# Kernel optimization log

Measured on AMD Instinct MI355X. Metric: run time of the kernel, lower is better.

Reference implementation:

```python
import jax, jax.numpy as jnp
import numpy as np
from jax import lax

# ---- config (matches init_kwargs) ----
B, S = 8, 256
WIDTH, LEVELS, STATE, PARAM = 32, 3, 1, 1
WSIZE = (64, 64)
PAD = 1  # padding//2 with padding=2

# ---- db6 filters (pywt ordering) ----
L = 12
DEC_LO = np.array([-0.00107730108499558, 0.004777257511010651, 0.0005538422009938016,
                   -0.031582039318031156, 0.02752286553001629, 0.09750160558707936,
                   -0.12976686756709563, -0.22626469396516913, 0.3152503517092432,
                   0.7511339080215775, 0.4946238903983854, 0.11154074335008017],
                  dtype=np.float32)
REC_LO = DEC_LO[::-1].copy()
REC_HI = ((-1.0) ** np.arange(L)).astype(np.float32) * DEC_LO
DEC_HI = REC_HI[::-1].copy()
# correlation kernels: analysis = flipped dec filters (= rec), synthesis = flipped rec (= dec)
KA = jnp.asarray(np.stack([REC_LO, REC_HI]))   # [2, L]
KS = jnp.asarray(np.stack([DEC_LO, DEC_HI]))   # [2, L]


def dwt1d(x, axis):
    """Single-level analysis along axis (2 or 3) of NCHW x; symmetric pad + stride-2 conv.
    Matches pytorch_wavelets afb1d (symmetric mode, even N)."""
    b, c = x.shape[0], x.shape[1]
    pads = [(0, 0)] * 4
    pads[axis] = (L - 2, L - 2)
    xp = jnp.pad(x, pads, mode='symmetric')
    xr = xp.reshape((b * c, 1) + xp.shape[2:])
    if axis == 2:
        k = KA.reshape(2, 1, L, 1); strides = (2, 1)
    else:
        k = KA.reshape(2, 1, 1, L); strides = (1, 2)
    y = lax.conv_general_dilated(xr, k, strides, 'VALID')  # [b*c, 2, H', W']
    y = y.reshape((b, c, 2) + y.shape[2:])
    return y[:, :, 0], y[:, :, 1]


def idwt1d(lo, hi, axis):
    """Single-level synthesis along axis: zero-upsample (lhs_dilation=2) + conv, crop L-2.
    Matches pytorch_wavelets sfb1d (conv_transpose stride 2, padding L-2)."""
    b, c = lo.shape[0], lo.shape[1]
    x = jnp.stack([lo, hi], axis=2).reshape((b * c, 2) + lo.shape[2:])
    if axis == 2:
        k = KS.reshape(1, 2, L, 1); ld = (2, 1); pad = ((1, 1), (0, 0))
    else:
        k = KS.reshape(1, 2, 1, L); ld = (1, 2); pad = ((0, 0), (1, 1))
    y = lax.conv_general_dilated(x, k, (1, 1), pad, lhs_dilation=ld)  # len = 2N-L+2
    return y.reshape((b, c) + y.shape[2:])


def afb2d(x):
    xl, xh = dwt1d(x, 3)
    ll, lh = dwt1d(xl, 2)
    hl, hh = dwt1d(xh, 2)
    return ll, jnp.stack([lh, hl, hh], axis=2)  # [B,C,3,H',W']


def sfb2d(ll, yh):
    lh, hl, hh = yh[:, :, 0], yh[:, :, 1], yh[:, :, 2]
    xl = idwt1d(ll, lh, 2)
    xh = idwt1d(hl, hh, 2)
    return idwt1d(xl, xh, 3)


def interp_bilinear(w, Ho, Wo):
    """F.interpolate(mode='bilinear', align_corners=False) on [I,O,h,w]."""
    h, wd = w.shape[2], w.shape[3]
    if (h, wd) == (Ho, Wo):
        return w
    def coords(n_out, n_in):
        scale = n_in / n_out
        s = jnp.maximum((jnp.arange(n_out, dtype=jnp.float32) + 0.5) * scale - 0.5, 0.0)
        i0 = jnp.minimum(jnp.floor(s).astype(jnp.int32), n_in - 1)
        i1 = jnp.minimum(i0 + 1, n_in - 1)
        t = jnp.clip(s - i0.astype(jnp.float32), 0.0, 1.0)
        return i0, i1, t
    y0, y1, ty = coords(Ho, h)
    x0, x1, tx = coords(Wo, wd)
    wr = w[:, :, y0, :] * (1.0 - ty)[None, None, :, None] + w[:, :, y1, :] * ty[None, None, :, None]
    return wr[:, :, :, x0] * (1.0 - tx) + wr[:, :, :, x1] * tx


def wavelet_conv(x, w):
    """WaveletConv2d.forward: J-level DWT, per-subband channel mix, IDWT."""
    orig = x.shape
    ll, highs = x, []
    for _ in range(LEVELS):
        ll, yh = afb2d(ll)
        highs.append(yh)
    wi = interp_bilinear(w, ll.shape[-2], ll.shape[-1])
    out = jnp.einsum('bixy,ioxy->boxy', ll, wi)
    out_h = []
    for h in highs:
        # torch code interpolates weights to input.shape[-3:-1] == (3, Hj) and broadcasts over W
        whi = interp_bilinear(w, h.shape[-3], h.shape[-2])
        out_h.append(jnp.einsum('bixyz,ioxy->boxyz', h, whi))
    for h in reversed(out_h):
        out = out[:, :, :h.shape[-2], :h.shape[-1]]
        out = sfb2d(out, h)
    return out[:, :, :orig[2], :orig[3]]


def wno2d(u, par, x, y, fc0_w, fc0_b, wc_w, pw_w, pw_b, fc1_w, fc1_b, fc2_w, fc2_b):
    b, s0, s1 = u.shape[0], u.shape[1], u.shape[2]
    gridx = jnp.broadcast_to(x[:, :, None, None], (b, s0, s1, 1))
    gridy = jnp.broadcast_to(y[:, None, :, None], (b, s0, s1, 1))
    h = jnp.concatenate([u, par, gridx, gridy], axis=-1)      # [B,S0,S1,4]
    h = h @ fc0_w.T + fc0_b                                   # [B,S0,S1,width]
    h = jnp.transpose(h, (0, 3, 1, 2))                        # NCHW
    h = jnp.pad(h, ((0, 0), (0, 0), (PAD, PAD), (PAD, PAD)), mode='reflect')
    for i in range(4):
        u1 = wavelet_conv(h, wc_w[i])
        u2 = jnp.einsum('bixy,oi->boxy', h, pw_w[i]) + pw_b[i][None, :, None, None]
        h = u1 + u2
        if i < 3:
            h = jax.nn.gelu(h, approximate=False)
    h = h[:, :, PAD:-PAD, PAD:-PAD]
    h = jnp.transpose(h, (0, 2, 3, 1))
    h = jax.nn.gelu(h @ fc1_w.T + fc1_b, approximate=False)
    return h @ fc2_w.T + fc2_b                                # [B,S0,S1,state]


def setup_inputs() -> dict:
    key = jax.random.key(0)
    ks = jax.random.split(key, 16)
    f32 = jnp.float32
    scale = 1.0 / (WIDTH * WIDTH)
    return {
        'u': jax.random.normal(ks[0], (B, S, S, STATE), f32),
        'par': jax.random.normal(ks[1], (B, S, S, PARAM), f32),
        'x': jax.random.uniform(ks[2], (B, S), f32),
        'y': jax.random.uniform(ks[3], (B, S), f32),
        'fc0_w': 0.3 * jax.random.normal(ks[4], (WIDTH, STATE + PARAM + 2), f32),
        'fc0_b': jnp.zeros((WIDTH,), f32),
        'wc_w': scale * jax.random.uniform(ks[5], (4, WIDTH, WIDTH) + WSIZE, f32),
        'pw_w': (1.0 / np.sqrt(WIDTH)) * jax.random.normal(ks[6], (4, WIDTH, WIDTH), f32),
        'pw_b': jnp.zeros((4, WIDTH), f32),
        'fc1_w': (1.0 / np.sqrt(WIDTH)) * jax.random.normal(ks[7], (128, WIDTH), f32),
        'fc1_b': jnp.zeros((128,), f32),
        'fc2_w': (1.0 / np.sqrt(128.0)) * jax.random.normal(ks[8], (STATE, 128), f32),
        'fc2_b': jnp.zeros((STATE,), f32),
    }


def reference(u, par, x, y, fc0_w, fc0_b, wc_w, pw_w, pw_b, fc1_w, fc1_b, fc2_w, fc2_b):
    return wno2d(u, par, x, y, fc0_w, fc0_b, wc_w, pw_w, pw_b, fc1_w, fc1_b, fc2_w, fc2_b)
```

## Files before the change

### kernel.cpp

```cpp
#include <hip/hip_runtime.h>
#include <math.h>

#define W0f  (-0.00107730108499558f)
#define W1f  (0.004777257511010651f)
#define W2f  (0.0005538422009938016f)
#define W3f  (-0.031582039318031156f)
#define W4f  (0.02752286553001629f)
#define W5f  (0.09750160558707936f)
#define W6f  (-0.12976686756709563f)
#define W7f  (-0.22626469396516913f)
#define W8f  (0.3152503517092432f)
#define W9f  (0.7511339080215775f)
#define W10f (0.4946238903983854f)
#define W11f (0.11154074335008017f)

__constant__ float cKA0[12] = {W11f,W10f,W9f,W8f,W7f,W6f,W5f,W4f,W3f,W2f,W1f,W0f};
__constant__ float cKA1[12] = {W0f,-W1f,W2f,-W3f,W4f,-W5f,W6f,-W7f,W8f,-W9f,W10f,-W11f};
__constant__ float cKS0[12] = {W0f,W1f,W2f,W3f,W4f,W5f,W6f,W7f,W8f,W9f,W10f,W11f};
__constant__ float cKS1[12] = {-W11f,W10f,-W9f,W8f,-W7f,W6f,-W5f,W4f,-W3f,W2f,-W1f,W0f};

#define S1c 134
#define S2c 72
#define S3c 41
#define A3c 1681
#define N1c 4596736UL
#define N2c 1327104UL
#define N3c 430336UL
#define PLc 2480128UL

__device__ __forceinline__ float gelu_f(float x) {
    float z  = x * 0.70710678118654752440f;
    float az = fabsf(z);
    float t  = __builtin_amdgcn_rcpf(1.0f + 0.3275911f * az);
    float p  = t * (0.254829592f + t * (-0.284496736f + t * (1.421413741f +
               t * (-1.453152027f + t * 1.061405429f))));
    float e  = __expf(-az * az);
    float er = copysignf(1.0f - p * e, z);
    return 0.5f * x * (1.0f + er);
}

__device__ __forceinline__ int xcd_swizzle() {
    int bid = blockIdx.x;
    return (bid & 7) * ((int)gridDim.x >> 3) + (bid >> 3);
}

__global__ __launch_bounds__(256) void dwt2d(
    const float* __restrict__ in, float* __restrict__ ll, float* __restrict__ lh,
    float* __restrict__ hl, float* __restrict__ hh, int H, int W, int Ho, int Wo,
    int tilesX, int tilesY) {
    int wg  = xcd_swizzle();
    int tpc = tilesX * tilesY;
    int c   = wg / tpc, rem = wg % tpc;
    int ty0 = (rem / tilesX) * 16;
    int tx0 = (rem % tilesX) * 16;
    const float* img = in + (size_t)c * H * W;
    __shared__ float sIn[42][45];
    __shared__ float rlo[42][17];
    __shared__ float rhi[42][17];
    int tid = threadIdx.x;
    for (int idx = tid; idx < 42 * 42; idx += 256) {
        int r = idx / 42, q = idx % 42;
        int gy = 2 * ty0 - 10 + r;
        int gx = 2 * tx0 - 10 + q;
        gy = gy < 0 ? -1 - gy : (gy >= H ? 2 * H - 1 - gy : gy);
        gx = gx < 0 ? -1 - gx : (gx >= W ? 2 * W - 1 - gx : gx);
        sIn[r][q] = img[gy * W + gx];
    }
    __syncthreads();
    for (int idx = tid; idx < 42 * 16; idx += 256) {
        int r = idx / 16, j = idx % 16;
        float alo = 0.f, ahi = 0.f;
        #pragma unroll
        for (int t = 0; t < 12; t++) {
            float v = sIn[r][2 * j + t];
            alo += v * cKA0[t];
            ahi += v * cKA1[t];
        }
        rlo[r][j] = alo; rhi[r][j] = ahi;
    }
    __syncthreads();
    int jy = tid / 16, jx = tid % 16;
    int oy = ty0 + jy, ox = tx0 + jx;
    if (oy < Ho && ox < Wo) {
        float a0 = 0.f, a1 = 0.f, a2 = 0.f, a3 = 0.f;
        #pragma unroll
        for (int t = 0; t < 12; t++) {
            float vl = rlo[2 * jy + t][jx];
            float vh = rhi[2 * jy + t][jx];
            a0 += vl * cKA0[t]; a1 += vl * cKA1[t];
            a2 += vh * cKA0[t]; a3 += vh * cKA1[t];
        }
        size_t o = (size_t)c * Ho * Wo + (size_t)oy * Wo + ox;
        ll[o] = a0; lh[o] = a1; hl[o] = a2; hh[o] = a3;
    }
}

__global__ __launch_bounds__(256) void dwt2d_fc0(
    const float* __restrict__ u, const float* __restrict__ par,
    const float* __restrict__ xg, const float* __restrict__ yg,
    const float* __restrict__ fw, const float* __restrict__ fb,
    float* __restrict__ ll, float* __restrict__ lh,
    float* __restrict__ hl, float* __restrict__ hh) {
    const int Hd = 258, S = 256, Ho = S1c, Wo = S1c, tilesX = 9;
    int wg  = xcd_swizzle();
    int tpc = tilesX * tilesX;
    int c   = wg / tpc, rem = wg % tpc;
    int b   = c >> 5, o = c & 31;
    int ty0 = (rem / tilesX) * 16;
    int tx0 = (rem % tilesX) * 16;
    float w0 = fw[o*4], w1 = fw[o*4+1], w2 = fw[o*4+2], w3 = fw[o*4+3], bv = fb[o];
    __shared__ float sIn[42][45];
    __shared__ float rlo[42][17];
    __shared__ float rhi[42][17];
    int tid = threadIdx.x;
    for (int idx = tid; idx < 42 * 42; idx += 256) {
        int r = idx / 42, q = idx % 42;
        int gy = 2 * ty0 - 10 + r;
        int gx = 2 * tx0 - 10 + q;
        gy = gy < 0 ? -1 - gy : (gy >= Hd ? 2 * Hd - 1 - gy : gy);
        gx = gx < 0 ? -1 - gx : (gx >= Hd ? 2 * Hd - 1 - gx : gx);
        int iy = gy - 1; iy = iy < 0 ? -iy : (iy >= S ? 2 * S - 2 - iy : iy);
        int ix = gx - 1; ix = ix < 0 ? -ix : (ix >= S ? 2 * S - 2 - ix : ix);
        float vu = u  [(b * S + iy) * S + ix];
        float vp = par[(b * S + iy) * S + ix];
        sIn[r][q] = w0 * vu + w1 * vp + w2 * xg[b * S + iy] + w3 * yg[b * S + ix] + bv;
    }
    __syncthreads();
    for (int idx = tid; idx < 42 * 16; idx += 256) {
        int r = idx / 16, j = idx % 16;
        float alo = 0.f, ahi = 0.f;
        #pragma unroll
        for (int t = 0; t < 12; t++) {
            float v = sIn[r][2 * j + t];
            alo += v * cKA0[t];
            ahi += v * cKA1[t];
        }
        rlo[r][j] = alo; rhi[r][j] = ahi;
    }
    __syncthreads();
    int jy = tid / 16, jx = tid % 16;
    int oy = ty0 + jy, ox = tx0 + jx;
    if (oy < Ho && ox < Wo) {
        float a0 = 0.f, a1 = 0.f, a2 = 0.f, a3 = 0.f;
        #pragma unroll
        for (int t = 0; t < 12; t++) {
            float vl = rlo[2 * jy + t][jx];
            float vh = rhi[2 * jy + t][jx];
            a0 += vl * cKA0[t]; a1 += vl * cKA1[t];
            a2 += vh * cKA0[t]; a3 += vh * cKA1[t];
        }
        size_t oo = (size_t)c * Ho * Wo + (size_t)oy * Wo + ox;
        ll[oo] = a0; lh[oo] = a1; hl[oo] = a2; hh[oo] = a3;
    }
}

__global__ __launch_bounds__(256) void idwt2d(
    const float* __restrict__ ll, const float* __restrict__ lh,
    const float* __restrict__ hl, const float* __restrict__ hh,
    float* __restrict__ out, const float* __restrict__ pb,
    int h, int w, int Oh, int Ow, int do_gelu, int tilesX, int tilesY) {
    int wg  = xcd_swizzle();
    int tpc = tilesX * tilesY;
    int c   = wg / tpc, rem = wg % tpc;
    int my0 = (rem / tilesX) * 16;
    int nx0 = (rem % tilesX) * 16;
    __shared__ float sll[21][22], slh[21][22], shl[21][22], shh[21][22];
    __shared__ float sxl[32][22], sxh[32][22];
    int tid = threadIdx.x;
    size_t cb = (size_t)c * h * w;
    float bias = pb ? pb[c & 31] : 0.f;
    for (int idx = tid; idx < 21 * 21; idx += 256) {
        int r = idx / 21, q = idx % 21;
        int gy = min(my0 + r, h - 1);
        int gx = min(nx0 + q, w - 1);
        size_t g = cb + (size_t)gy * w + gx;
        sll[r][q] = ll[g]; slh[r][q] = lh[g];
        shl[r][q] = hl[g]; shh[r][q] = hh[g];
    }
    __syncthreads();
    for (int idx = tid; idx < 32 * 21; idx += 256) {
        int r = idx / 21, q = idx % 21;
        int mp = r >> 1, p = r & 1;
        float al = 0.f, ah = 0.f;
        #pragma unroll
        for (int s = 0; s < 6; s++) {
            float k0 = cKS0[2 * s + 1 - p];
            float k1 = cKS1[2 * s + 1 - p];
            al += sll[mp + s][q] * k0 + slh[mp + s][q] * k1;
            ah += shl[mp + s][q] * k0 + shh[mp + s][q] * k1;
        }
        sxl[r][q] = al; sxh[r][q] = ah;
    }
    __syncthreads();
    for (int idx = tid; idx < 32 * 32; idx += 256) {
        int r = idx / 32, q2 = idx % 32;
        int np = q2 >> 1, q = q2 & 1;
        int oy = 2 * my0 + r, ox = 2 * nx0 + q2;
        if (oy < Oh && ox < Ow) {
            float a = bias;
            #pragma unroll
            for (int s = 0; s < 6; s++) {
                float k0 = cKS0[2 * s + 1 - q];
                float k1 = cKS1[2 * s + 1 - q];
                a += sxl[r][np + s] * k0 + sxh[r][np + s] * k1;
            }
            if (do_gelu) a = gelu_f(a);
            out[(size_t)c * Oh * Ow + (size_t)oy * Ow + ox] = a;
        }
    }
}

__global__ __launch_bounds__(256) void transpose_all(
    const float* __restrict__ w, float* __restrict__ wT) {
    __shared__ float t[64][65];
    int l  = blockIdx.y >> 4;
    int by = (blockIdx.y & 15) * 64;
    int bx = blockIdx.x * 64;
    const float* wl = w  + (size_t)l * 4194304;
    float* wTl      = wT + (size_t)l * 4194304;
    int tid = threadIdx.x;
    for (int idx = tid; idx < 4096; idx += 256) {
        int r = idx >> 6, q = idx & 63;
        t[r][q] = wl[(size_t)(by + r) * 4096 + bx + q];
    }
    __syncthreads();
    for (int idx = tid; idx < 4096; idx += 256) {
        int r = idx >> 6, q = idx & 63;
        wTl[(size_t)(bx + r) * 1024 + by + q] = t[q][r];
    }
}

__global__ __launch_bounds__(256) void interp4(
    const float* __restrict__ wT, const float* __restrict__ pw,
    float* __restrict__ wout) {
    int l = blockIdx.y;
    const float* wTl = wT + (size_t)l * 4194304;
    const float* pwl = pw + (size_t)l * 1024;
    float* base = wout + (size_t)l * PLc;
    __shared__ float spw[1024];
    int tid = threadIdx.x;
    for (int k = tid; k < 1024; k += 256) spw[k] = pwl[(k & 31) * 32 + (k >> 5)];
    __syncthreads();
    int bId = blockIdx.x;
    float* dst; int Ho, Wo, p;
    if (bId < A3c)                          { dst = base;                                 Ho = S3c; Wo = S3c; p = bId; }
    else if (bId < A3c + 3 * S1c)           { dst = base + A3c * 1024;                    Ho = 3;   Wo = S1c; p = bId - A3c; }
    else if (bId < A3c + 3 * (S1c + S2c))   { dst = base + (A3c + 3 * S1c) * 1024;        Ho = 3;   Wo = S2c; p = bId - A3c - 3 * S1c; }
    else                                    { dst = base + (A3c + 3 * (S1c + S2c)) * 1024; Ho = 3;  Wo = S3c; p = bId - A3c - 3 * (S1c + S2c); }
    int y = p / Wo, x = p % Wo;
    float sy = fmaxf((y + 0.5f) * (64.0f / Ho) - 0.5f, 0.0f);
    int y0 = min((int)sy, 63), y1 = min(y0 + 1, 63);
    float ty = fminf(sy - (float)y0, 1.0f);
    float sx = fmaxf((x + 0.5f) * (64.0f / Wo) - 0.5f, 0.0f);
    int x0 = min((int)sx, 63), x1 = min(x0 + 1, 63);
    float tx = fminf(sx - (float)x0, 1.0f);
    float c00 = (1.f - ty) * (1.f - tx), c01 = (1.f - ty) * tx;
    float c10 = ty * (1.f - tx),         c11 = ty * tx;
    const float4* s00 = (const float4*)(wTl + (size_t)(y0 * 64 + x0) * 1024);
    const float4* s01 = (const float4*)(wTl + (size_t)(y0 * 64 + x1) * 1024);
    const float4* s10 = (const float4*)(wTl + (size_t)(y1 * 64 + x0) * 1024);
    const float4* s11 = (const float4*)(wTl + (size_t)(y1 * 64 + x1) * 1024);
    float4* op = (float4*)(dst + (size_t)p * 1024);
    int k = tid;
    float4 a = s00[k], b = s01[k], c = s10[k], d = s11[k];
    float4 pw4 = *(const float4*)&spw[k * 4];
    float4 r;
    r.x = c00*a.x + c01*b.x + c10*c.x + c11*d.x + pw4.x;
    r.y = c00*a.y + c01*b.y + c10*c.y + c11*d.y + pw4.y;
    r.z = c00*a.z + c01*b.z + c10*c.z + c11*d.z + pw4.z;
    r.w = c00*a.w + c01*b.w + c10*c.w + c11*d.w + pw4.w;
    op[k] = r;
}

__global__ __launch_bounds__(256) void mix_all(
    float* __restrict__ ll3, float* __restrict__ lh3,
    float* __restrict__ lh2, float* __restrict__ lh1,
    const float* __restrict__ wl) {
    const float* wll = wl;
    const float* wh1 = wl + A3c * 1024;
    const float* wh2 = wh1 + 3 * S1c * 1024;
    const float* wh3 = wh2 + 3 * S2c * 1024;
    __shared__ float sw[1024];
    __shared__ float sv[256];
    int tid = threadIdx.x;
    int bid = blockIdx.x;
    if (bid < A3c) {
        const float* wb = wll + (size_t)bid * 1024;
        for (int k = tid; k < 1024; k += 256) sw[k] = wb[k];
        int b = tid >> 5, i = tid & 31;
        sv[tid] = ll3[((size_t)(b * 32 + i)) * A3c + bid];
        __syncthreads();
        float acc = 0.f;
        #pragma unroll
        for (int k = 0; k < 32; k++) acc += sv[b * 32 + k] * sw[k * 32 + i];
        ll3[((size_t)(b * 32 + i)) * A3c + bid] = acc;
        return;
    }
    int t = bid - A3c;
    float* hb; const float* wb; int Hs, Ws, s, y, xb; size_t bstride;
    if (t < 2 * S3c * 3) {
        Hs = Ws = S3c; bstride = N3c;
        int per = 2 * S3c; s = t / per; int r = t % per; y = r / 2; xb = r % 2;
        hb = lh3; wb = wh3;
    } else if ((t -= 2 * S3c * 3) < 3 * S2c * 3) {
        Hs = Ws = S2c; bstride = N2c;
        int per = 3 * S2c; s = t / per; int r = t % per; y = r / 3; xb = r % 3;
        hb = lh2; wb = wh2;
    } else {
        t -= 3 * S2c * 3;
        Hs = Ws = S1c; bstride = N1c;
        int per = 5 * S1c; s = t / per; int r = t % per; y = r / 5; xb = r % 5;
        hb = lh1; wb = wh1;
    }
    hb += (size_t)s * bstride;
    wb += ((size_t)s * Hs + y) * 1024;
    for (int k = tid; k < 1024; k += 256) sw[k] = wb[k];
    __syncthreads();
    int q = xb * 256 + tid;
    if (q >= 8 * Ws) return;
    int b = q / Ws, x = q % Ws;
    size_t base = ((size_t)(b * 32) * Hs + y) * Ws + x;
    size_t cs = (size_t)Hs * Ws;
    float acc[32];
    #pragma unroll
    for (int o = 0; o < 32; o++) acc[o] = 0.f;
    for (int i = 0; i < 32; i++) {
        float v = hb[base + (size_t)i * cs];
        #pragma unroll
        for (int o4 = 0; o4 < 8; o4++) {
            float4 w4 = *(const float4*)&sw[i * 32 + o4 * 4];
            acc[o4*4+0] += v * w4.x; acc[o4*4+1] += v * w4.y;
            acc[o4*4+2] += v * w4.z; acc[o4*4+3] += v * w4.w;
        }
    }
    #pragma unroll
    for (int o = 0; o < 32; o++) hb[base + (size_t)o * cs] = acc[o];
}

__global__ __launch_bounds__(256) void head_k(
    const float* __restrict__ h, const float* __restrict__ w1, const float* __restrict__ b1,
    const float* __restrict__ w2, const float* __restrict__ b2, float* __restrict__ out) {
    __shared__ float sw1[4096];
    __shared__ float sb1[128];
    __shared__ float sw2[128];
    int tid = threadIdx.x;
    for (int k = tid; k < 4096; k += 256) sw1[k] = w1[k];
    if (tid < 128) { sb1[tid] = b1[tid]; sw2[tid] = w2[tid]; }
    __syncthreads();
    const int Hp = 258;
    const int QP = 262144;
    int g0 = blockIdx.x * 256 + tid;
    float in[2][32];
    #pragma unroll
    for (int p = 0; p < 2; p++) {
        int gid = g0 + p * QP;
        int b = gid >> 16, r = gid & 65535;
        int yy = r >> 8, xx = r & 255;
        size_t base = (size_t)b * 32 * Hp * Hp + (size_t)(yy + 1) * Hp + (xx + 1);
        #pragma unroll
        for (int i = 0; i < 32; i++) in[p][i] = h[base + (size_t)i * Hp * Hp];
    }
    float acc0 = 0.f, acc1 = 0.f;
    for (int j = 0; j < 128; j++) {
        float h0 = sb1[j], h1 = h0;
        #pragma unroll
        for (int i4 = 0; i4 < 8; i4++) {
            float4 wv = *(const float4*)&sw1[j * 32 + i4 * 4];
            h0 += wv.x * in[0][i4*4+0] + wv.y * in[0][i4*4+1] + wv.z * in[0][i4*4+2] + wv.w * in[0][i4*4+3];
            h1 += wv.x * in[1][i4*4+0] + wv.y * in[1][i4*4+1] + wv.z * in[1][i4*4+2] + wv.w * in[1][i4*4+3];
        }
        float w2j = sw2[j];
        acc0 += w2j * gelu_f(h0);
        acc1 += w2j * gelu_f(h1);
    }
    float b2v = b2[0];
    out[g0     ] = acc0 + b2v;
    out[g0 + QP] = acc1 + b2v;
}

extern "C" void kernel_launch(void* const* d_in, const int* in_sizes, int n_in,
                              void* d_out, int out_size, void* d_ws, size_t ws_size,
                              hipStream_t stream) {
    (void)in_sizes; (void)n_in; (void)out_size;
    const float* u    = (const float*)d_in[0];
    const float* par  = (const float*)d_in[1];
    const float* xg   = (const float*)d_in[2];
    const float* yg   = (const float*)d_in[3];
    const float* fc0w = (const float*)d_in[4];
    const float* fc0b = (const float*)d_in[5];
    const float* wcw  = (const float*)d_in[6];
    const float* pww  = (const float*)d_in[7];
    const float* pwb  = (const float*)d_in[8];
    const float* fc1w = (const float*)d_in[9];
    const float* fc1b = (const float*)d_in[10];
    const float* fc2w = (const float*)d_in[11];
    const float* fc2b = (const float*)d_in[12];
    float* out = (float*)d_out;
    float* ws  = (float*)d_ws;

    const int Hp = 258;
    const size_t HW = (size_t)Hp * Hp;
    const size_t NH = 256 * HW;
    const int S1 = S1c, S2 = S2c, S3 = S3c;
    const size_t N1 = N1c, N2 = N2c, N3 = N3c;

    float* H   = ws;
    float* ll1 = H   + NH;
    float* lh1 = ll1 + N1;
    float* hl1 = lh1 + N1;
    float* hh1 = hl1 + N1;
    float* ll2 = hh1 + N1;
    float* lh2 = ll2 + N2;
    float* hl2 = lh2 + N2;
    float* hh2 = hl2 + N2;
    float* ll3 = hh2 + N2;
    float* lh3 = ll3 + N3;
    float* hl3 = lh3 + N3;
    float* hh3 = hl3 + N3;
    float* w4  = hh3 + N3;
    size_t needed = (size_t)(w4 + 4 * PLc - ws) * sizeof(float);
    if (ws_size < needed) return;
    float* wTall = lh1;

    const int tX1 = 9, tX2 = 5, tX3 = 3;
    const int iX3 = 3, iX2 = 5, iX1 = 9;

    transpose_all<<<dim3(64, 64), 256, 0, stream>>>(wcw, wTall);
    int nInterp = A3c + 3 * (S1 + S2 + S3);
    interp4<<<dim3(nInterp, 4), 256, 0, stream>>>(wTall, pww, w4);

    const int nMix = A3c + 2 * S3 * 3 + 3 * S2 * 3 + 5 * S1 * 3;

    for (int l = 0; l < 4; l++) {
        const float* wl = w4 + (size_t)l * PLc;

        if (l == 0) {
            dwt2d_fc0<<<tX1 * tX1 * 256, 256, 0, stream>>>(
                u, par, xg, yg, fc0w, fc0b, ll1, lh1, hl1, hh1);
        } else {
            dwt2d<<<tX1 * tX1 * 256, 256, 0, stream>>>(
                H, ll1, lh1, hl1, hh1, Hp, Hp, S1, S1, tX1, tX1);
        }
        dwt2d<<<tX2 * tX2 * 256, 256, 0, stream>>>(
            ll1, ll2, lh2, hl2, hh2, S1, S1, S2, S2, tX2, tX2);
        dwt2d<<<tX3 * tX3 * 256, 256, 0, stream>>>(
            ll2, ll3, lh3, hl3, hh3, S2, S2, S3, S3, tX3, tX3);

        mix_all<<<nMix, 256, 0, stream>>>(ll3, lh3, lh2, lh1, wl);

        idwt2d<<<iX3 * iX3 * 256, 256, 0, stream>>>(
            ll3, lh3, hl3, hh3, ll2, nullptr, S3, S3, S2, S2, 0, iX3, iX3);
        idwt2d<<<iX2 * iX2 * 256, 256, 0, stream>>>(
            ll2, lh2, hl2, hh2, ll1, nullptr, S2, S2, S1, S1, 0, iX2, iX2);
        idwt2d<<<iX1 * iX1 * 256, 256, 0, stream>>>(
            ll1, lh1, hl1, hh1, H, pwb + (size_t)l * 32, S1, S1, Hp, Hp,
            (l < 3) ? 1 : 0, iX1, iX1);
    }

    head_k<<<(8 * 256 * 256 / 2 + 255) / 256, 256, 0, stream>>>(H, fc1w, fc1b, fc2w, fc2b, out);
}
```

Measured before the change: 1.114 ms.

## Fuse mid-level wavelet stages into one cooperative persistent kernel with grid syncs

Merges the level-2/3 DWTs, the spectral mixing and the level-3/2 inverse DWTs into a single cooperative kernel. It uses grid-wide syncs between stages and grid-stride loops over the work items, so five launches per layer become one. This is meant to remove launch overhead and the idle gaps between the many small kernels. A fallback to separate launches runs if the cooperative launch fails. Separately, the head kernel now handles four pixels per thread instead of two, reusing each weight load over more pixels at the cost of extra registers.

```diff
diff --git a/kernel.cpp b/kernel.cpp
--- a/kernel.cpp
+++ b/kernel.cpp
@@ -1,4 +1,5 @@
 #include <hip/hip_runtime.h>
+#include <hip/hip_cooperative_groups.h>
 #include <math.h>
 
 #define W0f  (-0.00107730108499558f)
@@ -44,19 +45,19 @@
     return (bid & 7) * ((int)gridDim.x >> 3) + (bid >> 3);
 }
 
-__global__ __launch_bounds__(256) void dwt2d(
+
+__device__ __forceinline__ void dwt_body(
     const float* __restrict__ in, float* __restrict__ ll, float* __restrict__ lh,
-    float* __restrict__ hl, float* __restrict__ hh, int H, int W, int Ho, int Wo,
-    int tilesX, int tilesY) {
-    int wg  = xcd_swizzle();
-    int tpc = tilesX * tilesY;
+    float* __restrict__ hl, float* __restrict__ hh,
+    int H, int W, int Ho, int Wo, int tilesX, int wg, float* smem) {
+    float (*sIn)[45] = (float(*)[45])smem;
+    float (*rlo)[17] = (float(*)[17])(smem + 1890);
+    float (*rhi)[17] = (float(*)[17])(smem + 2604);
+    int tpc = tilesX * tilesX;
     int c   = wg / tpc, rem = wg % tpc;
     int ty0 = (rem / tilesX) * 16;
     int tx0 = (rem % tilesX) * 16;
     const float* img = in + (size_t)c * H * W;
-    __shared__ float sIn[42][45];
-    __shared__ float rlo[42][17];
-    __shared__ float rhi[42][17];
     int tid = threadIdx.x;
     for (int idx = tid; idx < 42 * 42; idx += 256) {
         int r = idx / 42, q = idx % 42;
@@ -93,6 +94,170 @@
         size_t o = (size_t)c * Ho * Wo + (size_t)oy * Wo + ox;
         ll[o] = a0; lh[o] = a1; hl[o] = a2; hh[o] = a3;
     }
+}
+
+__device__ __forceinline__ void idwt_body(
+    const float* __restrict__ ll, const float* __restrict__ lh,
+    const float* __restrict__ hl, const float* __restrict__ hh,
+    float* __restrict__ out, int h, int w, int Oh, int Ow, int tilesX,
+    int wg, float* smem) {
+    float (*sll)[22] = (float(*)[22])smem;
+    float (*slh)[22] = (float(*)[22])(smem + 462);
+    float (*shl)[22] = (float(*)[22])(smem + 924);
+    float (*shh)[22] = (float(*)[22])(smem + 1386);
+    float (*sxl)[22] = (float(*)[22])(smem + 1848);
+    float (*sxh)[22] = (float(*)[22])(smem + 2552);
+    int tpc = tilesX * tilesX;
+    int c   = wg / tpc, rem = wg % tpc;
+    int my0 = (rem / tilesX) * 16;
+    int nx0 = (rem % tilesX) * 16;
+    int tid = threadIdx.x;
+    size_t cb = (size_t)c * h * w;
+    for (int idx = tid; idx < 21 * 21; idx += 256) {
+        int r = idx / 21, q = idx % 21;
+        int gy = min(my0 + r, h - 1);
+        int gx = min(nx0 + q, w - 1);
+        size_t g = cb + (size_t)gy * w + gx;
+        sll[r][q] = ll[g]; slh[r][q] = lh[g];
+        shl[r][q] = hl[g]; shh[r][q] = hh[g];
+    }
+    __syncthreads();
+    for (int idx = tid; idx < 32 * 21; idx += 256) {
+        int r = idx / 21, q = idx % 21;
+        int mp = r >> 1, p = r & 1;
+        float al = 0.f, ah = 0.f;
+        #pragma unroll
+        for (int s = 0; s < 6; s++) {
+            float k0 = cKS0[2 * s + 1 - p];
+            float k1 = cKS1[2 * s + 1 - p];
+            al += sll[mp + s][q] * k0 + slh[mp + s][q] * k1;
+            ah += shl[mp + s][q] * k0 + shh[mp + s][q] * k1;
+        }
+        sxl[r][q] = al; sxh[r][q] = ah;
+    }
+    __syncthreads();
+    for (int idx = tid; idx < 32 * 32; idx += 256) {
+        int r = idx / 32, q2 = idx % 32;
+        int np = q2 >> 1, q = q2 & 1;
+        int oy = 2 * my0 + r, ox = 2 * nx0 + q2;
+        if (oy < Oh && ox < Ow) {
+            float a = 0.f;
+            #pragma unroll
+            for (int s = 0; s < 6; s++) {
+                float k0 = cKS0[2 * s + 1 - q];
+                float k1 = cKS1[2 * s + 1 - q];
+                a += sxl[r][np + s] * k0 + sxh[r][np + s] * k1;
+            }
+            out[(size_t)c * Oh * Ow + (size_t)oy * Ow + ox] = a;
+        }
+    }
+}
+
+__device__ __forceinline__ void mix_body(
+    float* __restrict__ ll3, float* __restrict__ lh3,
+    float* __restrict__ lh2, float* __restrict__ lh1,
+    const float* __restrict__ wl, int bid, float* smem) {
+    float* sw = smem;
+    float* sv = smem + 1024;
+    const float* wll = wl;
+    const float* wh1 = wl + A3c * 1024;
+    const float* wh2 = wh1 + 3 * S1c * 1024;
+    const float* wh3 = wh2 + 3 * S2c * 1024;
+    int tid = threadIdx.x;
+    if (bid < A3c) {
+        const float* wb = wll + (size_t)bid * 1024;
+        for (int k = tid; k < 1024; k += 256) sw[k] = wb[k];
+        int b = tid >> 5, i = tid & 31;
+        sv[tid] = ll3[((size_t)(b * 32 + i)) * A3c + bid];
+        __syncthreads();
+        float acc = 0.f;
+        #pragma unroll
+        for (int k = 0; k < 32; k++) acc += sv[b * 32 + k] * sw[k * 32 + i];
+        ll3[((size_t)(b * 32 + i)) * A3c + bid] = acc;
+        return;
+    }
+    int t = bid - A3c;
+    float* hb; const float* wb; int Hs, Ws, s, y, xb; size_t bstride;
+    if (t < 2 * S3c * 3) {
+        Hs = Ws = S3c; bstride = N3c;
+        int per = 2 * S3c; s = t / per; int r = t % per; y = r / 2; xb = r % 2;
+        hb = lh3; wb = wh3;
+    } else if ((t -= 2 * S3c * 3) < 3 * S2c * 3) {
+        Hs = Ws = S2c; bstride = N2c;
+        int per = 3 * S2c; s = t / per; int r = t % per; y = r / 3; xb = r % 3;
+        hb = lh2; wb = wh2;
+    } else {
+        t -= 3 * S2c * 3;
+        Hs = Ws = S1c; bstride = N1c;
+        int per = 5 * S1c; s = t / per; int r = t % per; y = r / 5; xb = r % 5;
+        hb = lh1; wb = wh1;
+    }
+    hb += (size_t)s * bstride;
+    wb += ((size_t)s * Hs + y) * 1024;
+    for (int k = tid; k < 1024; k += 256) sw[k] = wb[k];
+    __syncthreads();
+    int q = xb * 256 + tid;
+    if (q < 8 * Ws) {
+        int b = q / Ws, x = q % Ws;
+        size_t base = ((size_t)(b * 32) * Hs + y) * Ws + x;
+        size_t cs = (size_t)Hs * Ws;
+        float acc[32];
+        #pragma unroll
+        for (int o = 0; o < 32; o++) acc[o] = 0.f;
+        for (int i = 0; i < 32; i++) {
+            float v = hb[base + (size_t)i * cs];
+            #pragma unroll
+            for (int o4 = 0; o4 < 8; o4++) {
+                float4 w4 = *(const float4*)&sw[i * 32 + o4 * 4];
+                acc[o4*4+0] += v * w4.x; acc[o4*4+1] += v * w4.y;
+                acc[o4*4+2] += v * w4.z; acc[o4*4+3] += v * w4.w;
+            }
+        }
+        #pragma unroll
+        for (int o = 0; o < 32; o++) hb[base + (size_t)o * cs] = acc[o];
+    }
+}
+
+__global__ __launch_bounds__(256, 4) void mid_layer(
+    float* b1, float* ll2, float* lh2, float* hl2, float* hh2,
+    float* ll3, float* lh3, float* hl3, float* hh3, const float* wl) {
+    __shared__ float smem[3328];
+    cooperative_groups::grid_group grid = cooperative_groups::this_grid();
+    float* ll1 = b1;
+    float* lh1 = b1 + N1c;
+    for (int w = blockIdx.x; w < 6400; w += gridDim.x) {
+        dwt_body(ll1, ll2, lh2, hl2, hh2, S1c, S1c, S2c, S2c, 5, w, smem);
+        __syncthreads();
+    }
+    grid.sync();
+    for (int w = blockIdx.x; w < 2304; w += gridDim.x) {
+        dwt_body(ll2, ll3, lh3, hl3, hh3, S2c, S2c, S3c, S3c, 3, w, smem);
+        __syncthreads();
+    }
+    grid.sync();
+    for (int w = blockIdx.x; w < 4585; w += gridDim.x) {
+        mix_body(ll3, lh3, lh2, lh1, wl, w, smem);
+        __syncthreads();
+    }
+    grid.sync();
+    for (int w = blockIdx.x; w < 2304; w += gridDim.x) {
+        idwt_body(ll3, lh3, hl3, hh3, ll2, S3c, S3c, S2c, S2c, 3, w, smem);
+        __syncthreads();
+    }
+    grid.sync();
+    for (int w = blockIdx.x; w < 6400; w += gridDim.x) {
+        idwt_body(ll2, lh2, hl2, hh2, ll1, S2c, S2c, S1c, S1c, 5, w, smem);
+        __syncthreads();
+    }
+}
+
+
+__global__ __launch_bounds__(256) void dwt2d(
+    const float* __restrict__ in, float* __restrict__ ll, float* __restrict__ lh,
+    float* __restrict__ hl, float* __restrict__ hh, int H, int W, int Ho, int Wo,
+    int tilesX) {
+    __shared__ float smem[3328];
+    dwt_body(in, ll, lh, hl, hh, H, W, Ho, Wo, tilesX, xcd_swizzle(), smem);
 }
 
 __global__ __launch_bounds__(256) void dwt2d_fc0(
@@ -158,9 +323,9 @@
     const float* __restrict__ ll, const float* __restrict__ lh,
     const float* __restrict__ hl, const float* __restrict__ hh,
     float* __restrict__ out, const float* __restrict__ pb,
-    int h, int w, int Oh, int Ow, int do_gelu, int tilesX, int tilesY) {
+    int h, int w, int Oh, int Ow, int do_gelu, int tilesX) {
     int wg  = xcd_swizzle();
-    int tpc = tilesX * tilesY;
+    int tpc = tilesX * tilesX;
     int c   = wg / tpc, rem = wg % tpc;
     int my0 = (rem / tilesX) * 16;
     int nx0 = (rem % tilesX) * 16;
@@ -210,6 +375,14 @@
     }
 }
 
+__global__ __launch_bounds__(256) void mix_all(
+    float* __restrict__ ll3, float* __restrict__ lh3,
+    float* __restrict__ lh2, float* __restrict__ lh1,
+    const float* __restrict__ wl) {
+    __shared__ float smem[1280];
+    mix_body(ll3, lh3, lh2, lh1, wl, blockIdx.x, smem);
+}
+
 __global__ __launch_bounds__(256) void transpose_all(
     const float* __restrict__ w, float* __restrict__ wT) {
     __shared__ float t[64][65];
@@ -243,10 +416,10 @@
     __syncthreads();
     int bId = blockIdx.x;
     float* dst; int Ho, Wo, p;
-    if (bId < A3c)                          { dst = base;                                 Ho = S3c; Wo = S3c; p = bId; }
-    else if (bId < A3c + 3 * S1c)           { dst = base + A3c * 1024;                    Ho = 3;   Wo = S1c; p = bId - A3c; }
-    else if (bId < A3c + 3 * (S1c + S2c))   { dst = base + (A3c + 3 * S1c) * 1024;        Ho = 3;   Wo = S2c; p = bId - A3c - 3 * S1c; }
-    else                                    { dst = base + (A3c + 3 * (S1c + S2c)) * 1024; Ho = 3;  Wo = S3c; p = bId - A3c - 3 * (S1c + S2c); }
+    if (bId < A3c)                          { dst = base;                                  Ho = S3c; Wo = S3c; p = bId; }
+    else if (bId < A3c + 3 * S1c)           { dst = base + A3c * 1024;                     Ho = 3;   Wo = S1c; p = bId - A3c; }
+    else if (bId < A3c + 3 * (S1c + S2c))   { dst = base + (A3c + 3 * S1c) * 1024;         Ho = 3;   Wo = S2c; p = bId - A3c - 3 * S1c; }
+    else                                    { dst = base + (A3c + 3 * (S1c + S2c)) * 1024; Ho = 3;   Wo = S3c; p = bId - A3c - 3 * (S1c + S2c); }
     int y = p / Wo, x = p % Wo;
     float sy = fmaxf((y + 0.5f) * (64.0f / Ho) - 0.5f, 0.0f);
     int y0 = min((int)sy, 63), y1 = min(y0 + 1, 63);
@@ -272,71 +445,6 @@
     op[k] = r;
 }
 
-__global__ __launch_bounds__(256) void mix_all(
-    float* __restrict__ ll3, float* __restrict__ lh3,
-    float* __restrict__ lh2, float* __restrict__ lh1,
-    const float* __restrict__ wl) {
-    const float* wll = wl;
-    const float* wh1 = wl + A3c * 1024;
-    const float* wh2 = wh1 + 3 * S1c * 1024;
-    const float* wh3 = wh2 + 3 * S2c * 1024;
-    __shared__ float sw[1024];
-    __shared__ float sv[256];
-    int tid = threadIdx.x;
-    int bid = blockIdx.x;
-    if (bid < A3c) {
-        const float* wb = wll + (size_t)bid * 1024;
-        for (int k = tid; k < 1024; k += 256) sw[k] = wb[k];
-        int b = tid >> 5, i = tid & 31;
-        sv[tid] = ll3[((size_t)(b * 32 + i)) * A3c + bid];
-        __syncthreads();
-        float acc = 0.f;
-        #pragma unroll
-        for (int k = 0; k < 32; k++) acc += sv[b * 32 + k] * sw[k * 32 + i];
-        ll3[((size_t)(b * 32 + i)) * A3c + bid] = acc;
-        return;
-    }
-    int t = bid - A3c;
-    float* hb; const float* wb; int Hs, Ws, s, y, xb; size_t bstride;
-    if (t < 2 * S3c * 3) {
-        Hs = Ws = S3c; bstride = N3c;
-        int per = 2 * S3c; s = t / per; int r = t % per; y = r / 2; xb = r % 2;
-        hb = lh3; wb = wh3;
-    } else if ((t -= 2 * S3c * 3) < 3 * S2c * 3) {
-        Hs = Ws = S2c; bstride = N2c;
-        int per = 3 * S2c; s = t / per; int r = t % per; y = r / 3; xb = r % 3;
-        hb = lh2; wb = wh2;
-    } else {
-        t -= 3 * S2c * 3;
-        Hs = Ws = S1c; bstride = N1c;
-        int per = 5 * S1c; s = t / per; int r = t % per; y = r / 5; xb = r % 5;
-        hb = lh1; wb = wh1;
-    }
-    hb += (size_t)s * bstride;
-    wb += ((size_t)s * Hs + y) * 1024;
-    for (int k = tid; k < 1024; k += 256) sw[k] = wb[k];
-    __syncthreads();
-    int q = xb * 256 + tid;
-    if (q >= 8 * Ws) return;
-    int b = q / Ws, x = q % Ws;
-    size_t base = ((size_t)(b * 32) * Hs + y) * Ws + x;
-    size_t cs = (size_t)Hs * Ws;
-    float acc[32];
-    #pragma unroll
-    for (int o = 0; o < 32; o++) acc[o] = 0.f;
-    for (int i = 0; i < 32; i++) {
-        float v = hb[base + (size_t)i * cs];
-        #pragma unroll
-        for (int o4 = 0; o4 < 8; o4++) {
-            float4 w4 = *(const float4*)&sw[i * 32 + o4 * 4];
-            acc[o4*4+0] += v * w4.x; acc[o4*4+1] += v * w4.y;
-            acc[o4*4+2] += v * w4.z; acc[o4*4+3] += v * w4.w;
-        }
-    }
-    #pragma unroll
-    for (int o = 0; o < 32; o++) hb[base + (size_t)o * cs] = acc[o];
-}
-
 __global__ __launch_bounds__(256) void head_k(
     const float* __restrict__ h, const float* __restrict__ w1, const float* __restrict__ b1,
     const float* __restrict__ w2, const float* __restrict__ b2, float* __restrict__ out) {
@@ -348,11 +456,11 @@
     if (tid < 128) { sb1[tid] = b1[tid]; sw2[tid] = w2[tid]; }
     __syncthreads();
     const int Hp = 258;
-    const int QP = 262144;
+    const int QP = 131072;
     int g0 = blockIdx.x * 256 + tid;
-    float in[2][32];
+    float in[4][32];
     #pragma unroll
-    for (int p = 0; p < 2; p++) {
+    for (int p = 0; p < 4; p++) {
         int gid = g0 + p * QP;
         int b = gid >> 16, r = gid & 65535;
         int yy = r >> 8, xx = r & 255;
@@ -360,22 +468,29 @@
         #pragma unroll
         for (int i = 0; i < 32; i++) in[p][i] = h[base + (size_t)i * Hp * Hp];
     }
-    float acc0 = 0.f, acc1 = 0.f;
+    float acc0 = 0.f, acc1 = 0.f, acc2 = 0.f, acc3 = 0.f;
     for (int j = 0; j < 128; j++) {
-        float h0 = sb1[j], h1 = h0;
+        float bj = sb1[j];
+        float h0 = bj, h1 = bj, h2 = bj, h3 = bj;
         #pragma unroll
         for (int i4 = 0; i4 < 8; i4++) {
             float4 wv = *(const float4*)&sw1[j * 32 + i4 * 4];
             h0 += wv.x * in[0][i4*4+0] + wv.y * in[0][i4*4+1] + wv.z * in[0][i4*4+2] + wv.w * in[0][i4*4+3];
             h1 += wv.x * in[1][i4*4+0] + wv.y * in[1][i4*4+1] + wv.z * in[1][i4*4+2] + wv.w * in[1][i4*4+3];
+            h2 += wv.x * in[2][i4*4+0] + wv.y * in[2][i4*4+1] + wv.z * in[2][i4*4+2] + wv.w * in[2][i4*4+3];
+            h3 += wv.x * in[3][i4*4+0] + wv.y * in[3][i4*4+1] + wv.z * in[3][i4*4+2] + wv.w * in[3][i4*4+3];
         }
         float w2j = sw2[j];
         acc0 += w2j * gelu_f(h0);
         acc1 += w2j * gelu_f(h1);
+        acc2 += w2j * gelu_f(h2);
+        acc3 += w2j * gelu_f(h3);
     }
     float b2v = b2[0];
-    out[g0     ] = acc0 + b2v;
-    out[g0 + QP] = acc1 + b2v;
+    out[g0          ] = acc0 + b2v;
+    out[g0 +     QP ] = acc1 + b2v;
+    out[g0 + 2 * QP ] = acc2 + b2v;
+    out[g0 + 3 * QP ] = acc3 + b2v;
 }
 
 extern "C" void kernel_launch(void* const* d_in, const int* in_sizes, int n_in,
@@ -405,11 +520,8 @@
     const size_t N1 = N1c, N2 = N2c, N3 = N3c;
 
     float* H   = ws;
-    float* ll1 = H   + NH;
-    float* lh1 = ll1 + N1;
-    float* hl1 = lh1 + N1;
-    float* hh1 = hl1 + N1;
-    float* ll2 = hh1 + N1;
+    float* b1  = H   + NH;
+    float* ll2 = b1  + 4 * N1;
     float* lh2 = ll2 + N2;
     float* hl2 = lh2 + N2;
     float* hh2 = hl2 + N2;
@@ -420,10 +532,7 @@
     float* w4  = hh3 + N3;
     size_t needed = (size_t)(w4 + 4 * PLc - ws) * sizeof(float);
     if (ws_size < needed) return;
-    float* wTall = lh1;
-
-    const int tX1 = 9, tX2 = 5, tX3 = 3;
-    const int iX3 = 3, iX2 = 5, iX1 = 9;
+    float* wTall = b1 + N1;
 
     transpose_all<<<dim3(64, 64), 256, 0, stream>>>(wcw, wTall);
     int nInterp = A3c + 3 * (S1 + S2 + S3);
@@ -435,27 +544,35 @@
         const float* wl = w4 + (size_t)l * PLc;
 
         if (l == 0) {
-            dwt2d_fc0<<<tX1 * tX1 * 256, 256, 0, stream>>>(
-                u, par, xg, yg, fc0w, fc0b, ll1, lh1, hl1, hh1);
+            dwt2d_fc0<<<9 * 9 * 256, 256, 0, stream>>>(
+                u, par, xg, yg, fc0w, fc0b, b1, b1 + N1, b1 + 2 * N1, b1 + 3 * N1);
         } else {
-            dwt2d<<<tX1 * tX1 * 256, 256, 0, stream>>>(
-                H, ll1, lh1, hl1, hh1, Hp, Hp, S1, S1, tX1, tX1);
-        }
-        dwt2d<<<tX2 * tX2 * 256, 256, 0, stream>>>(
-            ll1, ll2, lh2, hl2, hh2, S1, S1, S2, S2, tX2, tX2);
-        dwt2d<<<tX3 * tX3 * 256, 256, 0, stream>>>(
-            ll2, ll3, lh3, hl3, hh3, S2, S2, S3, S3, tX3, tX3);
-
-        mix_all<<<nMix, 256, 0, stream>>>(ll3, lh3, lh2, lh1, wl);
-
-        idwt2d<<<iX3 * iX3 * 256, 256, 0, stream>>>(
-            ll3, lh3, hl3, hh3, ll2, nullptr, S3, S3, S2, S2, 0, iX3, iX3);
-        idwt2d<<<iX2 * iX2 * 256, 256, 0, stream>>>(
-            ll2, lh2, hl2, hh2, ll1, nullptr, S2, S2, S1, S1, 0, iX2, iX2);
-        idwt2d<<<iX1 * iX1 * 256, 256, 0, stream>>>(
-            ll1, lh1, hl1, hh1, H, pwb + (size_t)l * 32, S1, S1, Hp, Hp,
-            (l < 3) ? 1 : 0, iX1, iX1);
-    }
-
-    head_k<<<(8 * 256 * 256 / 2 + 255) / 256, 256, 0, stream>>>(H, fc1w, fc1b, fc2w, fc2b, out);
-}
+            dwt2d<<<9 * 9 * 256, 256, 0, stream>>>(
+                H, b1, b1 + N1, b1 + 2 * N1, b1 + 3 * N1, Hp, Hp, S1, S1, 9);
+        }
+
+        {
+            void* args[] = {(void*)&b1, (void*)&ll2, (void*)&lh2, (void*)&hl2, (void*)&hh2,
+                            (void*)&ll3, (void*)&lh3, (void*)&hl3, (void*)&hh3, (void*)&wl};
+            hipError_t e = hipLaunchCooperativeKernel((void*)mid_layer, dim3(1024), dim3(256),
+                                                      args, 0, stream);
+            if (e != hipSuccess) {
+                dwt2d<<<5 * 5 * 256, 256, 0, stream>>>(
+                    b1, ll2, lh2, hl2, hh2, S1, S1, S2, S2, 5);
+                dwt2d<<<3 * 3 * 256, 256, 0, stream>>>(
+                    ll2, ll3, lh3, hl3, hh3, S2, S2, S3, S3, 3);
+                mix_all<<<nMix, 256, 0, stream>>>(ll3, lh3, lh2, b1 + N1, wl);
+                idwt2d<<<3 * 3 * 256, 256, 0, stream>>>(
+                    ll3, lh3, hl3, hh3, ll2, nullptr, S3, S3, S2, S2, 0, 3);
+                idwt2d<<<5 * 5 * 256, 256, 0, stream>>>(
+                    ll2, lh2, hl2, hh2, b1, nullptr, S2, S2, S1, S1, 0, 5);
+            }
+        }
+
+        idwt2d<<<9 * 9 * 256, 256, 0, stream>>>(
+            b1, b1 + N1, b1 + 2 * N1, b1 + 3 * N1, H, pwb + (size_t)l * 32,
+            S1, S1, Hp, Hp, (l < 3) ? 1 : 0, 9);
+    }
+
+    head_k<<<(8 * 256 * 256 / 4 + 255) / 256, 256, 0, stream>>>(H, fc1w, fc1b, fc2w, fc2b, out);
+}
```

Result: slower. 3.202 ms (+187.4%).
